# Optimization experiments

Measured on AMD Instinct MI355X. Metric: run time of the kernel, lower is better.

The kernel has to match this reference:

```python
import jax, jax.numpy as jnp
import numpy as np


def _nearest_down(x, oh, ow):
    # torch F.interpolate(mode='nearest'): src_idx = floor(dst_idx * in/out)
    ih, iw = x.shape[-2], x.shape[-1]
    hi = jnp.floor(jnp.arange(oh) * (ih / oh)).astype(jnp.int32)
    wi = jnp.floor(jnp.arange(ow) * (iw / ow)).astype(jnp.int32)
    return x[..., hi, :][..., :, wi]


def setup_inputs() -> dict:
    key = jax.random.key(0)
    k1, k2, k3, k4 = jax.random.split(key, 4)
    B, Cf, Hf, Wf = 8, 256, 128, 128   # encoder feature map (stride 4)
    HL, WL = 512, 512                  # label / logit resolution
    C_OLD, NUM_CLASSES = 16, 21
    return {
        "outputs": jnp.zeros((1,), jnp.float32),        # overwritten in original forward
        "outputs_old": jax.random.normal(k1, (B, C_OLD, HL, WL), jnp.float32),
        "features": jax.random.normal(k2, (B, Cf, Hf, Wf), jnp.float32),
        "features_old": jnp.zeros((1,), jnp.float32),   # unused by this branch
        "labels": jax.random.randint(k3, (B, HL, WL), 0, NUM_CLASSES),
        "prototypes": jax.random.normal(k4, (NUM_CLASSES, Cf), jnp.float32),
        "classes_old": 16,
        "incremental_step": 1,
    }


def reference(outputs, outputs_old, features, features_old, labels, prototypes,
              classes_old, incremental_step):
    # Default branch: val=False, sequential=False, loss_de_prototypes_sumafter=False.
    if incremental_step == 0:
        return jnp.asarray(0.0, jnp.float32)
    B, C, H, W = features.shape
    # downsample labels to feature resolution (nearest)
    labels_down = _nearest_down(labels[:, None, :, :], H, W)      # [B,1,H,W] int
    bgr_mask = labels_down == 0
    # old-model pseudo-labels, masked to background of current labels
    pred_old = jnp.argmax(outputs_old, axis=1, keepdims=True)      # [B,1,HL,WL]
    pred_old_down = _nearest_down(pred_old, H, W)                  # [B,1,H,W]
    pseudo = jnp.where(bgr_mask, pred_old_down, 0)                 # [B,1,H,W]

    ids = pseudo.reshape(-1)                                       # [N]
    feats = jnp.transpose(features, (0, 2, 3, 1)).reshape(-1, C)   # [N,C]
    proto = jax.lax.stop_gradient(prototypes)                      # .detach()

    # per-pixel MSE (mean over channels) vs the prototype of its pseudo-class
    per_pix = jnp.mean(jnp.square(feats - proto[ids]), axis=-1)    # [N]

    sums = jax.ops.segment_sum(per_pix, ids, num_segments=classes_old)
    counts = jax.ops.segment_sum(jnp.ones_like(per_pix), ids, num_segments=classes_old)
    # mean over pixels of each present class; absent classes contribute 0
    per_class = jnp.where(counts > 0, sums / jnp.maximum(counts, 1.0), 0.0)
    # class 0 is excluded (cl_present drops background)
    return jnp.sum(per_class[1:])
```

## Files before the change

kernel.cpp:

```cpp
#include <hip/hip_runtime.h>

#define BB    8
#define CF    256
#define HF    128
#define WF    128
#define HLBL  512
#define WLBL  512
#define COLD  16
#define NCLS  21
#define PSTR  257


__global__ __launch_bounds__(256) void proto_loss_main(
    const float* __restrict__ outputs_old,
    const float* __restrict__ features,
    const int*   __restrict__ labels,
    const float* __restrict__ prototypes,
    float* __restrict__ gbins)
{
    __shared__ float sproto[NCLS * PSTR];
    __shared__ float spartial[8][WF];
    __shared__ int   sids[WF];
    __shared__ float ssum[16];
    __shared__ float scnt[16];

    const int t   = threadIdx.x;
    const int blk = blockIdx.x;
    const int b   = blk >> 7;
    const int h   = blk & (HF - 1);

    for (int i = t; i < NCLS * CF; i += 256) {
        int r = i >> 8;
        int c = i & (CF - 1);
        sproto[r * PSTR + c] = prototypes[i];
    }
    if (t < 16) { ssum[t] = 0.0f; scnt[t] = 0.0f; }

    if (t < WF) {
        const int w = t;
        int id = 0;
        const int lab = labels[(b * HLBL + h * 4) * WLBL + w * 4];
        if (lab == 0) {
            const float* po = outputs_old
                + ((size_t)b * COLD * HLBL + (size_t)h * 4) * WLBL + w * 4;
            float best = po[0];
            for (int c = 1; c < COLD; ++c) {
                float v = po[(size_t)c * HLBL * WLBL];
                if (v > best) { best = v; id = c; }
            }
        }
        sids[w] = id;
    }
    __syncthreads();

    const int w4    = (t & 31) * 4;
    const int c_off = t >> 5;
    const int id0 = sids[w4 + 0];
    const int id1 = sids[w4 + 1];
    const int id2 = sids[w4 + 2];
    const int id3 = sids[w4 + 3];
    const float* pr0 = &sproto[id0 * PSTR];
    const float* pr1 = &sproto[id1 * PSTR];
    const float* pr2 = &sproto[id2 * PSTR];
    const float* pr3 = &sproto[id3 * PSTR];

    const float* fbase = features + ((size_t)b * CF * HF + h) * WF + w4;

    float a0 = 0.f, a1 = 0.f, a2 = 0.f, a3 = 0.f;
    #pragma unroll 4
    for (int k = 0; k < 32; ++k) {
        const int c = k * 8 + c_off;
        const float4 f = *(const float4*)(fbase + (size_t)c * (HF * WF));
        float d0 = f.x - pr0[c]; a0 += d0 * d0;
        float d1 = f.y - pr1[c]; a1 += d1 * d1;
        float d2 = f.z - pr2[c]; a2 += d2 * d2;
        float d3 = f.w - pr3[c]; a3 += d3 * d3;
    }
    spartial[c_off][w4 + 0] = a0;
    spartial[c_off][w4 + 1] = a1;
    spartial[c_off][w4 + 2] = a2;
    spartial[c_off][w4 + 3] = a3;
    __syncthreads();

    if (t < WF) {
        float pp = 0.f;
        #pragma unroll
        for (int co = 0; co < 8; ++co) pp += spartial[co][t];
        pp *= (1.0f / CF);
        const int id = sids[t];
        atomicAdd(&ssum[id], pp);
        atomicAdd(&scnt[id], 1.0f);
    }
    __syncthreads();

    if (t < 16) {
        if (scnt[t] > 0.f) {
            atomicAdd(&gbins[t],      ssum[t]);
            atomicAdd(&gbins[16 + t], scnt[t]);
        }
    }
}

__global__ void proto_loss_final(const float* __restrict__ gbins,
                                 const int* __restrict__ classes_old,
                                 const int* __restrict__ inc_step,
                                 float* __restrict__ out)
{
    if (threadIdx.x == 0 && blockIdx.x == 0) {
        float r = 0.0f;
        if (*inc_step != 0) {
            int K = *classes_old;
            if (K > 16) K = 16;
            for (int id = 1; id < K; ++id) {
                float cnt = gbins[16 + id];
                if (cnt > 0.f) r += gbins[id] / cnt;
            }
        }
        out[0] = r;
    }
}

extern "C" void kernel_launch(void* const* d_in, const int* in_sizes, int n_in,
                              void* d_out, int out_size, void* d_ws, size_t ws_size,
                              hipStream_t stream)
{
    const float* outputs_old = (const float*)d_in[1];
    const float* features    = (const float*)d_in[2];
    const int*   labels      = (const int*)d_in[4];
    const float* prototypes  = (const float*)d_in[5];
    const int*   classes_old = (const int*)d_in[6];
    const int*   inc_step    = (const int*)d_in[7];

    float* gbins = (float*)d_ws;

    hipMemsetAsync(gbins, 0, 32 * sizeof(float), stream);

    dim3 grid(BB * HF);
    dim3 block(256);
    proto_loss_main<<<grid, block, 0, stream>>>(outputs_old, features, labels,
                                                prototypes, gbins);
    proto_loss_final<<<1, 64, 0, stream>>>(gbins, classes_old, inc_step,
                                           (float*)d_out);
}
```

Before: 270.7 us.

## Compute feature distances only for nonzero pseudo-label pixels via compacted list

```diff
diff --git a/kernel.cpp b/kernel.cpp
--- a/kernel.cpp
+++ b/kernel.cpp
@@ -1,119 +1,114 @@
 #include <hip/hip_runtime.h>
 
-#define BB    8
-#define CF    256
-#define HF    128
-#define WF    128
-#define HLBL  512
-#define WLBL  512
-#define COLD  16
-#define NCLS  21
-#define PSTR  257
+#define BB   8
+#define CF   256
+#define HF   128
+#define WF   128
+#define HL   512
+#define WL   512
+#define COLD 16
 
 
-__global__ __launch_bounds__(256) void proto_loss_main(
+__global__ __launch_bounds__(256) void proto_loss_sparse(
     const float* __restrict__ outputs_old,
     const float* __restrict__ features,
     const int*   __restrict__ labels,
     const float* __restrict__ prototypes,
-    float* __restrict__ gbins)
+    float* __restrict__ ws)
 {
-    __shared__ float sproto[NCLS * PSTR];
-    __shared__ float spartial[8][WF];
-    __shared__ int   sids[WF];
+    __shared__ int   plist[WF];
     __shared__ float ssum[16];
-    __shared__ float scnt[16];
+    __shared__ int   scnt[16];
+    __shared__ int   lcnt;
 
     const int t   = threadIdx.x;
     const int blk = blockIdx.x;
     const int b   = blk >> 7;
     const int h   = blk & (HF - 1);
 
-    for (int i = t; i < NCLS * CF; i += 256) {
-        int r = i >> 8;
-        int c = i & (CF - 1);
-        sproto[r * PSTR + c] = prototypes[i];
-    }
-    if (t < 16) { ssum[t] = 0.0f; scnt[t] = 0.0f; }
-
-    if (t < WF) {
-        const int w = t;
-        int id = 0;
-        const int lab = labels[(b * HLBL + h * 4) * WLBL + w * 4];
-        if (lab == 0) {
-            const float* po = outputs_old
-                + ((size_t)b * COLD * HLBL + (size_t)h * 4) * WLBL + w * 4;
-            float best = po[0];
-            for (int c = 1; c < COLD; ++c) {
-                float v = po[(size_t)c * HLBL * WLBL];
-                if (v > best) { best = v; id = c; }
-            }
-        }
-        sids[w] = id;
-    }
-    __syncthreads();
-
-    const int w4    = (t & 31) * 4;
-    const int c_off = t >> 5;
-    const int id0 = sids[w4 + 0];
-    const int id1 = sids[w4 + 1];
-    const int id2 = sids[w4 + 2];
-    const int id3 = sids[w4 + 3];
-    const float* pr0 = &sproto[id0 * PSTR];
-    const float* pr1 = &sproto[id1 * PSTR];
-    const float* pr2 = &sproto[id2 * PSTR];
-    const float* pr3 = &sproto[id3 * PSTR];
-
-    const float* fbase = features + ((size_t)b * CF * HF + h) * WF + w4;
-
-    float a0 = 0.f, a1 = 0.f, a2 = 0.f, a3 = 0.f;
-    #pragma unroll 4
-    for (int k = 0; k < 32; ++k) {
-        const int c = k * 8 + c_off;
-        const float4 f = *(const float4*)(fbase + (size_t)c * (HF * WF));
-        float d0 = f.x - pr0[c]; a0 += d0 * d0;
-        float d1 = f.y - pr1[c]; a1 += d1 * d1;
-        float d2 = f.z - pr2[c]; a2 += d2 * d2;
-        float d3 = f.w - pr3[c]; a3 += d3 * d3;
-    }
-    spartial[c_off][w4 + 0] = a0;
-    spartial[c_off][w4 + 1] = a1;
-    spartial[c_off][w4 + 2] = a2;
-    spartial[c_off][w4 + 3] = a3;
+    if (t < 16) { ssum[t] = 0.0f; scnt[t] = 0; }
+    if (t == 0) lcnt = 0;
     __syncthreads();
 
     if (t < WF) {
-        float pp = 0.f;
+        const int w   = t;
+        const int lab = labels[(b * HL + h * 4) * WL + w * 4];
+        if (lab == 0) {
+            const float* po = outputs_old
+                + ((size_t)(b * COLD) * HL + (size_t)(h * 4)) * WL + w * 4;
+            float best = po[0];
+            int   id   = 0;
+            #pragma unroll
+            for (int c = 1; c < COLD; ++c) {
+                float v = po[(size_t)c * (HL * WL)];
+                if (v > best) { best = v; id = c; }
+            }
+            if (id > 0) {
+                int pos = atomicAdd(&lcnt, 1);
+                plist[pos] = w | (id << 16);
+                atomicAdd(&scnt[id], 1);
+            }
+        }
+    }
+    __syncthreads();
+    const int m = lcnt;
+
+    const int wave = t >> 6;
+    const int lane = t & 63;
+    for (int p = wave; p < m; p += 4) {
+        const int e  = plist[p];
+        const int w  = e & 0xffff;
+        const int id = e >> 16;
+        const float* fb = features + ((size_t)(b * CF) * HF + h) * WF + w;
+        const float* pr = prototypes + id * CF;
+        float acc = 0.0f;
         #pragma unroll
-        for (int co = 0; co < 8; ++co) pp += spartial[co][t];
-        pp *= (1.0f / CF);
-        const int id = sids[t];
-        atomicAdd(&ssum[id], pp);
-        atomicAdd(&scnt[id], 1.0f);
+        for (int k = 0; k < 4; ++k) {
+            const int c = lane + 64 * k;
+            const float d = fb[(size_t)c * (HF * WF)] - pr[c];
+            acc += d * d;
+        }
+        #pragma unroll
+        for (int off = 32; off > 0; off >>= 1)
+            acc += __shfl_xor(acc, off, 64);
+        if (lane == 0)
+            atomicAdd(&ssum[id], acc * (1.0f / CF));
     }
     __syncthreads();
 
     if (t < 16) {
-        if (scnt[t] > 0.f) {
-            atomicAdd(&gbins[t],      ssum[t]);
-            atomicAdd(&gbins[16 + t], scnt[t]);
-        }
+        ws[blk * 32 + t]      = ssum[t];
+        ws[blk * 32 + 16 + t] = (float)scnt[t];
     }
 }
 
-__global__ void proto_loss_final(const float* __restrict__ gbins,
-                                 const int* __restrict__ classes_old,
-                                 const int* __restrict__ inc_step,
-                                 float* __restrict__ out)
+__global__ __launch_bounds__(256) void proto_loss_final(
+    const float* __restrict__ ws,
+    const int*   __restrict__ classes_old,
+    const int*   __restrict__ inc_step,
+    float* __restrict__ out)
 {
-    if (threadIdx.x == 0 && blockIdx.x == 0) {
+    __shared__ float red[8 * 32];
+    const int t   = threadIdx.x;
+    const int s   = t & 31;
+    const int grp = t >> 5;
+    float acc = 0.0f;
+    for (int i = grp; i < BB * HF; i += 8)
+        acc += ws[i * 32 + s];
+    red[grp * 32 + s] = acc;
+    __syncthreads();
+    if (t == 0) {
         float r = 0.0f;
         if (*inc_step != 0) {
             int K = *classes_old;
             if (K > 16) K = 16;
             for (int id = 1; id < K; ++id) {
-                float cnt = gbins[16 + id];
-                if (cnt > 0.f) r += gbins[id] / cnt;
+                float sum = 0.0f, cnt = 0.0f;
+                for (int g = 0; g < 8; ++g) {
+                    sum += red[g * 32 + id];
+                    cnt += red[g * 32 + 16 + id];
+                }
+                if (cnt > 0.0f) r += sum / cnt;
             }
         }
         out[0] = r;
@@ -131,14 +126,10 @@
     const int*   classes_old = (const int*)d_in[6];
     const int*   inc_step    = (const int*)d_in[7];
 
-    float* gbins = (float*)d_ws;
+    float* ws = (float*)d_ws;
 
-    hipMemsetAsync(gbins, 0, 32 * sizeof(float), stream);
-
-    dim3 grid(BB * HF);
-    dim3 block(256);
-    proto_loss_main<<<grid, block, 0, stream>>>(outputs_old, features, labels,
-                                                prototypes, gbins);
-    proto_loss_final<<<1, 64, 0, stream>>>(gbins, classes_old, inc_step,
-                                           (float*)d_out);
+    proto_loss_sparse<<<dim3(BB * HF), dim3(256), 0, stream>>>(
+        outputs_old, features, labels, prototypes, ws);
+    proto_loss_final<<<dim3(1), dim3(256), 0, stream>>>(
+        ws, classes_old, inc_step, (float*)d_out);
 }
```

Result: slower. 291.7 us (+7.8%).
